# Optimization experiments

Hardware: AMD Instinct MI355X
Metric: run time of the kernel (lower is better)

Reference implementation:

```python
import jax, jax.numpy as jnp
import numpy as np

B, S, DM, H = 4, 2048, 512, 8
HD = DM // H


def setup_inputs() -> dict:
    key = jax.random.key(0)
    ks = jax.random.split(key, 12)
    x = jax.random.normal(ks[0], (B, S, DM), dtype=jnp.float32)
    # causal lower-triangular mask [B, S, S]
    mask = jnp.broadcast_to(jnp.tril(jnp.ones((S, S), dtype=jnp.int32)), (B, S, S))
    # sorted irregular day offsets (trading-day-like), in days
    days_offset = jnp.sort(
        jax.random.uniform(ks[1], (B, S), dtype=jnp.float32) * 3000.0, axis=-1
    )
    scale = 1.0 / np.sqrt(DM)
    Wq = jax.random.normal(ks[2], (DM, DM), dtype=jnp.float32) * scale
    bq = jnp.zeros((DM,), dtype=jnp.float32)
    Wk = jax.random.normal(ks[3], (DM, DM), dtype=jnp.float32) * scale
    bk = jnp.zeros((DM,), dtype=jnp.float32)
    Wv = jax.random.normal(ks[4], (DM, DM), dtype=jnp.float32) * scale
    bv = jnp.zeros((DM,), dtype=jnp.float32)
    Wo = jax.random.normal(ks[5], (DM, DM), dtype=jnp.float32) * scale
    bo = jnp.zeros((DM,), dtype=jnp.float32)
    decay_rate = jnp.float32(0.1)
    return {
        "x": x, "mask": mask, "days_offset": days_offset,
        "Wq": Wq, "bq": bq, "Wk": Wk, "bk": bk,
        "Wv": Wv, "bv": bv, "Wo": Wo, "bo": bo,
        "decay_rate": decay_rate,
    }


def reference(x, mask, days_offset, Wq, bq, Wk, bk, Wv, bv, Wo, bo, decay_rate):
    b, s, _ = x.shape
    # projections (torch Linear: x @ W.T + b), split heads -> [b, h, s, hd]
    def proj(W, bias):
        return (x @ W.T + bias).reshape(b, s, H, HD).transpose(0, 2, 1, 3)
    q, k, v = proj(Wq, bq), proj(Wk, bk), proj(Wv, bv)
    scores = jnp.einsum("bhqd,bhkd->bhqk", q, k) / jnp.sqrt(jnp.float32(HD))
    # temporal decay: exp(-rate * |t_i - t_j|), broadcast over heads
    dist = jnp.abs(days_offset[:, :, None] - days_offset[:, None, :])  # [b,s,s]
    decay = jnp.exp(-decay_rate * dist)
    scores = scores * decay[:, None, :, :]
    scores = jnp.where(mask[:, None, :, :] == 0, -jnp.inf, scores)
    attn = jax.nn.softmax(scores, axis=-1)  # dropout p=0 (eval)
    out = jnp.einsum("bhqk,bhkd->bhqd", attn, v)
    out = out.transpose(0, 2, 1, 3).reshape(b, s, DM)
    return out @ Wo.T + bo
```

## Files before the change

kernel.cpp:

```cpp
#include <hip/hip_runtime.h>
#include <hip/hip_fp16.h>


#define S_LEN 2048
#define DMODEL 512
#define NH 8
#define HD 64

typedef _Float16 half8 __attribute__((ext_vector_type(8)));
typedef _Float16 half4 __attribute__((ext_vector_type(4)));
typedef float floatx4 __attribute__((ext_vector_type(4)));

__device__ __forceinline__ void gload16(const _Float16* g, _Float16* l) {
    __builtin_amdgcn_global_load_lds(
        (const __attribute__((address_space(1))) void*)g,
        (__attribute__((address_space(3))) void*)l, 16, 0, 0);
}

__global__ __launch_bounds__(256) void cast_f32_f16(
    const float* __restrict__ x,
    const float* __restrict__ Wq, const float* __restrict__ Wk,
    const float* __restrict__ Wv, const float* __restrict__ Wo,
    _Float16* __restrict__ xh, _Float16* __restrict__ Wh)
{
    int i = blockIdx.x * 256 + threadIdx.x;
    const float* src; _Float16* dst; int off;
    if (i < 1048576) { src = x; dst = xh; off = i; }
    else {
        int j = i - 1048576;
        int w = j >> 16;
        int within = j & 65535;
        src = (w == 0) ? Wq : (w == 1) ? Wk : (w == 2) ? Wv : Wo;
        dst = Wh + w * (DMODEL * DMODEL);
        off = within;
    }
    float4 v = ((const float4*)src)[off];
    half4 h;
    h.x = (_Float16)v.x; h.y = (_Float16)v.y; h.z = (_Float16)v.z; h.w = (_Float16)v.w;
    *(half4*)(dst + (size_t)off * 4) = h;
}

template <int MODE>
__global__ __launch_bounds__(256) void gemm_k(
    const _Float16* __restrict__ A, const _Float16* __restrict__ Wbase,
    const float* __restrict__ b0, const float* __restrict__ b1,
    const float* __restrict__ b2,
    _Float16* __restrict__ outh, float* __restrict__ outf)
{
    __shared__ _Float16 As[128 * 64];
    __shared__ _Float16 Ws[128 * 64];
    __shared__ char epbuf[MODE == 0 ? (4 * 16 * 72 * 2) : (4 * 16 * 68 * 4)];
    const int t = threadIdx.x;
    const int bm = blockIdx.x, bn = blockIdx.y, z = blockIdx.z;
    const _Float16* Wp = Wbase + (MODE == 0 ? z * (DMODEL * DMODEL) : 0);
    const float* bias = (MODE == 0) ? (z == 0 ? b0 : (z == 1 ? b1 : b2)) : b0;
    const int w = t >> 6, lane = t & 63, l15 = lane & 15, quad = lane >> 4;
    const int wrow = (w >> 1) * 64, wcol = (w & 1) * 64;
    const int lrow = lane >> 3;
    const int sw = (lane & 7) ^ lrow;

    floatx4 acc[4][4] = {};
    for (int kb = 0; kb < 8; ++kb) {
        __syncthreads();
        #pragma unroll
        for (int i = 0; i < 4; ++i) {
            int row0 = w * 32 + i * 8;
            gload16(A  + (size_t)(bm * 128 + row0 + lrow) * DMODEL + kb * 64 + sw * 8, &As[row0 * 64]);
            gload16(Wp + (size_t)(bn * 128 + row0 + lrow) * DMODEL + kb * 64 + sw * 8, &Ws[row0 * 64]);
        }
        __syncthreads();
        #pragma unroll
        for (int kk = 0; kk < 2; ++kk) {
            half8 af[4], bf[4];
            #pragma unroll
            for (int mt = 0; mt < 4; ++mt)
                af[mt] = *(const half8*)(&As[(wrow + mt * 16 + l15) * 64 + (((quad + 4 * kk) ^ (l15 & 7)) * 8)]);
            #pragma unroll
            for (int nt = 0; nt < 4; ++nt)
                bf[nt] = *(const half8*)(&Ws[(wcol + nt * 16 + l15) * 64 + (((quad + 4 * kk) ^ (l15 & 7)) * 8)]);
            #pragma unroll
            for (int mt = 0; mt < 4; ++mt)
                #pragma unroll
                for (int nt = 0; nt < 4; ++nt)
                    acc[mt][nt] = __builtin_amdgcn_mfma_f32_16x16x32_f16(af[mt], bf[nt], acc[mt][nt], 0, 0, 0);
        }
    }

    if (MODE == 0 && z == 2) {
        #pragma unroll
        for (int mt = 0; mt < 4; ++mt)
            #pragma unroll
            for (int nt = 0; nt < 4; ++nt) {
                int n = bn * 128 + wcol + nt * 16 + l15;
                float bvv = bias[n];
                int m0 = bm * 128 + wrow + mt * 16 + quad * 4;
                int b = m0 >> 11, s0 = m0 & 2047;
                int hh = n >> 6, hd = n & 63;
                half4 hv;
                #pragma unroll
                for (int r = 0; r < 4; ++r) hv[r] = (_Float16)(acc[mt][nt][r] + bvv);
                *(half4*)(outh + (size_t)2 * (8192 * 512) +
                          ((size_t)(b * NH + hh) * HD + hd) * S_LEN + s0) = hv;
            }
    } else {
        float bv4[4];
        #pragma unroll
        for (int nt = 0; nt < 4; ++nt) bv4[nt] = bias[bn * 128 + wcol + nt * 16 + l15];
        const int rr = lane >> 3, cc = (lane & 7) ^ rr;
        if (MODE == 0) {
            _Float16* Ep = (_Float16*)epbuf + w * (16 * 72);
            const int hq = (bn * 128 + wcol) >> 6;
            #pragma unroll
            for (int mt = 0; mt < 4; ++mt) {
                #pragma unroll
                for (int nt = 0; nt < 4; ++nt)
                    #pragma unroll
                    for (int r = 0; r < 4; ++r)
                        Ep[(quad * 4 + r) * 72 + nt * 16 + l15] = (_Float16)(acc[mt][nt][r] + bv4[nt]);
                #pragma unroll
                for (int i2 = 0; i2 < 2; ++i2) {
                    int row = i2 * 8 + rr;
                    half8 v = *(const half8*)(&Ep[row * 72 + cc * 8]);
                    int m = bm * 128 + wrow + mt * 16 + row;
                    int bb = m >> 11, ss = m & 2047;
                    *(half8*)(outh + (size_t)z * (8192 * 512) +
                              ((size_t)(bb * NH + hq) * S_LEN + ss) * HD + cc * 8) = v;
                }
            }
        } else {
            float* Epf = (float*)epbuf + w * (16 * 68);
            #pragma unroll
            for (int mt = 0; mt < 4; ++mt) {
                #pragma unroll
                for (int nt = 0; nt < 4; ++nt)
                    #pragma unroll
                    for (int r = 0; r < 4; ++r)
                        Epf[(quad * 4 + r) * 68 + nt * 16 + l15] = acc[mt][nt][r] + bv4[nt];
                #pragma unroll
                for (int i2 = 0; i2 < 4; ++i2) {
                    int row = (i2 & 1) * 8 + rr;
                    int ch = cc + (i2 >> 1) * 8;
                    float4 v = *(const float4*)(&Epf[row * 68 + ch * 4]);
                    int m = bm * 128 + wrow + mt * 16 + row;
                    *(float4*)(outf + (size_t)m * DMODEL + bn * 128 + wcol + ch * 4) = v;
                }
            }
        }
    }
}

__global__ __launch_bounds__(256, 2) void attn_k(
    const _Float16* __restrict__ Qh, const _Float16* __restrict__ Kh,
    const _Float16* __restrict__ Vt, const float* __restrict__ days,
    const float* __restrict__ rate_p, _Float16* __restrict__ Ah)
{
    __shared__ _Float16 Ks[2][64 * 64];
    __shared__ _Float16 Vs[2][64 * 64];
    __shared__ float    eks[2][64];
    __shared__ _Float16 Ps[4][16 * 64];

    const int pr = blockIdx.x, h = blockIdx.y, b = blockIdx.z;
    const int t = threadIdx.x, w = t >> 6, lane = t & 63, l15 = lane & 15, quad = lane >> 4;
    const float rate = rate_p[0];
    const size_t bhoff = (size_t)(b * NH + h) * (size_t)(S_LEN * HD);
    const _Float16* Qb = Qh + bhoff;
    const _Float16* Kb = Kh + bhoff;
    const _Float16* Vb = Vt + bhoff;
    const float* daysb = days + b * S_LEN;
    const int lrow = lane >> 3, sw = (lane & 7) ^ lrow;
    const int e7 = l15 & 7;

    auto stage = [&](int kt, int buf) {
        #pragma unroll
        for (int i = 0; i < 2; ++i) {
            int grp = w * 2 + i;
            int row = grp * 8 + lrow;
            gload16(Kb + (size_t)(kt * 64 + row) * HD + sw * 8, &Ks[buf][grp * 512]);
            gload16(Vb + (size_t)row * S_LEN + kt * 64 + sw * 8, &Vs[buf][grp * 512]);
        }
        if (w == 0) {
            float tk0 = daysb[kt * 64];
            float d = daysb[kt * 64 + lane];
            eks[buf][lane] = __expf(fminf(rate * (d - tk0), 80.f));
        }
    };

    auto run_phase = [&](int j, int par0, int nextj) -> int {
        const int qg = j * 64 + w * 16 + l15;
        half8 qf0 = *(const half8*)(Qb + (size_t)qg * HD + quad * 8);
        half8 qf1 = *(const half8*)(Qb + (size_t)qg * HD + 32 + quad * 8);
        const float tq = daysb[qg];
        floatx4 oacc[4] = {};
        float lacc = 0.f;

        for (int kt = 0; kt <= j; ++kt) {
            const int par = (par0 + kt) & 1;
            __syncthreads();
            if (kt < j) stage(kt + 1, par ^ 1);
            else if (nextj >= 0) stage(0, par ^ 1);
            const float tk0 = daysb[kt * 64];
            half8 kf[4][2];
            #pragma unroll
            for (int c = 0; c < 4; ++c)
                #pragma unroll
                for (int kk = 0; kk < 2; ++kk)
                    kf[c][kk] = *(const half8*)(&Ks[par][(c * 16 + l15) * 64 + (((quad + 4 * kk) ^ e7) * 8)]);
            floatx4 sc[4];
            #pragma unroll
            for (int c = 0; c < 4; ++c) {
                floatx4 z4 = {};
                z4 = __builtin_amdgcn_mfma_f32_16x16x32_f16(kf[c][0], qf0, z4, 0, 0, 0);
                sc[c] = __builtin_amdgcn_mfma_f32_16x16x32_f16(kf[c][1], qf1, z4, 0, 0, 0);
            }
            half8 vf[4][2];
            #pragma unroll
            for (int s4 = 0; s4 < 4; ++s4)
                #pragma unroll
                for (int kk = 0; kk < 2; ++kk)
                    vf[s4][kk] = *(const half8*)(&Vs[par][(s4 * 16 + l15) * 64 + (((quad + 4 * kk) ^ e7) * 8)]);
            floatx4 ekv[4];
            #pragma unroll
            for (int c = 0; c < 4; ++c)
                ekv[c] = *(const floatx4*)(&eks[par][c * 16 + quad * 4]);
            const float eq = 0.125f * __expf(-rate * (tq - tk0));
            const bool dg = (kt == j);
            #pragma unroll
            for (int c = 0; c < 4; ++c) {
                float pvv[4];
                #pragma unroll
                for (int r = 0; r < 4; ++r) {
                    float sv = sc[c][r] * (eq * ekv[c][r]);
                    float p = __expf(sv - 2.0f);
                    if (dg && (kt * 64 + c * 16 + quad * 4 + r) > qg) p = 0.f;
                    lacc += p;
                    pvv[r] = p;
                }
                half4 hv;
                hv.x = (_Float16)pvv[0]; hv.y = (_Float16)pvv[1];
                hv.z = (_Float16)pvv[2]; hv.w = (_Float16)pvv[3];
                *(half4*)(&Ps[w][l15 * 64 + (((2 * c + (quad >> 1)) ^ e7) * 8) + (quad & 1) * 4]) = hv;
            }
            half8 pf0 = *(const half8*)(&Ps[w][l15 * 64 + ((quad ^ e7) * 8)]);
            half8 pf1 = *(const half8*)(&Ps[w][l15 * 64 + (((4 + quad) ^ e7) * 8)]);
            #pragma unroll
            for (int s4 = 0; s4 < 4; ++s4) {
                oacc[s4] = __builtin_amdgcn_mfma_f32_16x16x32_f16(vf[s4][0], pf0, oacc[s4], 0, 0, 0);
                oacc[s4] = __builtin_amdgcn_mfma_f32_16x16x32_f16(vf[s4][1], pf1, oacc[s4], 0, 0, 0);
            }
        }

        float l = lacc;
        l += __shfl_xor(l, 16);
        l += __shfl_xor(l, 32);
        float linv = 1.0f / l;
        #pragma unroll
        for (int s4 = 0; s4 < 4; ++s4) {
            half4 hv;
            #pragma unroll
            for (int r = 0; r < 4; ++r) hv[r] = (_Float16)(oacc[s4][r] * linv);
            *(half4*)(Ah + ((size_t)(b * S_LEN) + qg) * DMODEL + h * HD + s4 * 16 + quad * 4) = hv;
        }
        return (par0 + j + 1) & 1;
    };

    const int j0 = pr, j1 = 31 - pr;
    stage(0, 0);
    int p1 = run_phase(j0, 0, j1);
    run_phase(j1, p1, -1);
}

extern "C" void kernel_launch(void* const* d_in, const int* in_sizes, int n_in,
                              void* d_out, int out_size, void* d_ws, size_t ws_size,
                              hipStream_t stream)
{
    const float* x    = (const float*)d_in[0];
    const float* days = (const float*)d_in[2];
    const float* Wq   = (const float*)d_in[3];
    const float* bq   = (const float*)d_in[4];
    const float* Wk   = (const float*)d_in[5];
    const float* bk   = (const float*)d_in[6];
    const float* Wv   = (const float*)d_in[7];
    const float* bv   = (const float*)d_in[8];
    const float* Wo   = (const float*)d_in[9];
    const float* bo   = (const float*)d_in[10];
    const float* rate = (const float*)d_in[11];
    float* out = (float*)d_out;

    _Float16* xh = (_Float16*)d_ws;
    _Float16* Wh = xh + 4194304;
    _Float16* Qh = Wh + 1048576;
    _Float16* Kh = Qh + 4194304;
    _Float16* Vh = Kh + 4194304;
    _Float16* Ah = Vh + 4194304;

    cast_f32_f16<<<5120, 256, 0, stream>>>(x, Wq, Wk, Wv, Wo, xh, Wh);

    dim3 g0(64, 4, 3);
    gemm_k<0><<<g0, 256, 0, stream>>>(xh, Wh, bq, bk, bv, Qh, nullptr);

    dim3 ga(16, NH, 4);
    attn_k<<<ga, 256, 0, stream>>>(Qh, Kh, Vh, days, rate, Ah);

    dim3 g1(64, 4, 1);
    gemm_k<1><<<g1, 256, 0, stream>>>(Ah, Wh + 3 * (DMODEL * DMODEL), bo, bo, bo, nullptr, out);
}
```

Baseline: 206.9 us.

## Fuse fp32-to-fp16 cast into GEMM staging and reorder attention grid

```diff
diff --git a/kernel.cpp b/kernel.cpp
--- a/kernel.cpp
+++ b/kernel.cpp
@@ -17,47 +17,36 @@
         (__attribute__((address_space(3))) void*)l, 16, 0, 0);
 }
 
-__global__ __launch_bounds__(256) void cast_f32_f16(
+__device__ __forceinline__ void stage_f32(
+    const float* __restrict__ src, _Float16* __restrict__ dstbase,
+    int row0, int lrow, int sw, int lane7, int kcol)
+{
+    const float* p = src + (size_t)(row0 + lrow) * DMODEL + kcol + sw * 8;
+    float4 a = *(const float4*)p;
+    float4 b = *(const float4*)(p + 4);
+    half8 h;
+    h[0] = (_Float16)a.x; h[1] = (_Float16)a.y; h[2] = (_Float16)a.z; h[3] = (_Float16)a.w;
+    h[4] = (_Float16)b.x; h[5] = (_Float16)b.y; h[6] = (_Float16)b.z; h[7] = (_Float16)b.w;
+    *(half8*)(dstbase + (row0 + lrow) * 64 + lane7 * 8) = h;
+}
+
+__global__ __launch_bounds__(256) void qkv_gemm(
     const float* __restrict__ x,
-    const float* __restrict__ Wq, const float* __restrict__ Wk,
-    const float* __restrict__ Wv, const float* __restrict__ Wo,
-    _Float16* __restrict__ xh, _Float16* __restrict__ Wh)
-{
-    int i = blockIdx.x * 256 + threadIdx.x;
-    const float* src; _Float16* dst; int off;
-    if (i < 1048576) { src = x; dst = xh; off = i; }
-    else {
-        int j = i - 1048576;
-        int w = j >> 16;
-        int within = j & 65535;
-        src = (w == 0) ? Wq : (w == 1) ? Wk : (w == 2) ? Wv : Wo;
-        dst = Wh + w * (DMODEL * DMODEL);
-        off = within;
-    }
-    float4 v = ((const float4*)src)[off];
-    half4 h;
-    h.x = (_Float16)v.x; h.y = (_Float16)v.y; h.z = (_Float16)v.z; h.w = (_Float16)v.w;
-    *(half4*)(dst + (size_t)off * 4) = h;
-}
-
-template <int MODE>
-__global__ __launch_bounds__(256) void gemm_k(
-    const _Float16* __restrict__ A, const _Float16* __restrict__ Wbase,
-    const float* __restrict__ b0, const float* __restrict__ b1,
-    const float* __restrict__ b2,
-    _Float16* __restrict__ outh, float* __restrict__ outf)
+    const float* __restrict__ Wq, const float* __restrict__ Wk, const float* __restrict__ Wv,
+    const float* __restrict__ bq, const float* __restrict__ bk, const float* __restrict__ bv,
+    _Float16* __restrict__ outh)
 {
     __shared__ _Float16 As[128 * 64];
     __shared__ _Float16 Ws[128 * 64];
-    __shared__ char epbuf[MODE == 0 ? (4 * 16 * 72 * 2) : (4 * 16 * 68 * 4)];
+    __shared__ _Float16 Ep[4][16 * 72];
     const int t = threadIdx.x;
     const int bm = blockIdx.x, bn = blockIdx.y, z = blockIdx.z;
-    const _Float16* Wp = Wbase + (MODE == 0 ? z * (DMODEL * DMODEL) : 0);
-    const float* bias = (MODE == 0) ? (z == 0 ? b0 : (z == 1 ? b1 : b2)) : b0;
+    const float* Wp = (z == 0) ? Wq : (z == 1) ? Wk : Wv;
+    const float* bias = (z == 0) ? bq : (z == 1) ? bk : bv;
     const int w = t >> 6, lane = t & 63, l15 = lane & 15, quad = lane >> 4;
     const int wrow = (w >> 1) * 64, wcol = (w & 1) * 64;
-    const int lrow = lane >> 3;
-    const int sw = (lane & 7) ^ lrow;
+    const int lrow = lane >> 3, lane7 = lane & 7;
+    const int sw = lane7 ^ lrow;
 
     floatx4 acc[4][4] = {};
     for (int kb = 0; kb < 8; ++kb) {
@@ -65,8 +54,8 @@
         #pragma unroll
         for (int i = 0; i < 4; ++i) {
             int row0 = w * 32 + i * 8;
-            gload16(A  + (size_t)(bm * 128 + row0 + lrow) * DMODEL + kb * 64 + sw * 8, &As[row0 * 64]);
-            gload16(Wp + (size_t)(bn * 128 + row0 + lrow) * DMODEL + kb * 64 + sw * 8, &Ws[row0 * 64]);
+            stage_f32(x  + (size_t)(bm * 128) * DMODEL, As, row0, lrow, sw, lane7, kb * 64);
+            stage_f32(Wp + (size_t)(bn * 128) * DMODEL, Ws, row0, lrow, sw, lane7, kb * 64);
         }
         __syncthreads();
         #pragma unroll
@@ -86,7 +75,7 @@
         }
     }
 
-    if (MODE == 0 && z == 2) {
+    if (z == 2) {
         #pragma unroll
         for (int mt = 0; mt < 4; ++mt)
             #pragma unroll
@@ -107,44 +96,88 @@
         #pragma unroll
         for (int nt = 0; nt < 4; ++nt) bv4[nt] = bias[bn * 128 + wcol + nt * 16 + l15];
         const int rr = lane >> 3, cc = (lane & 7) ^ rr;
-        if (MODE == 0) {
-            _Float16* Ep = (_Float16*)epbuf + w * (16 * 72);
-            const int hq = (bn * 128 + wcol) >> 6;
-            #pragma unroll
-            for (int mt = 0; mt < 4; ++mt) {
+        _Float16* E = Ep[w];
+        const int hq = (bn * 128 + wcol) >> 6;
+        #pragma unroll
+        for (int mt = 0; mt < 4; ++mt) {
+            #pragma unroll
+            for (int nt = 0; nt < 4; ++nt)
+                #pragma unroll
+                for (int r = 0; r < 4; ++r)
+                    E[(quad * 4 + r) * 72 + nt * 16 + l15] = (_Float16)(acc[mt][nt][r] + bv4[nt]);
+            #pragma unroll
+            for (int i2 = 0; i2 < 2; ++i2) {
+                int row = i2 * 8 + rr;
+                half8 v = *(const half8*)(&E[row * 72 + cc * 8]);
+                int m = bm * 128 + wrow + mt * 16 + row;
+                int bb = m >> 11, ss = m & 2047;
+                *(half8*)(outh + (size_t)z * (8192 * 512) +
+                          ((size_t)(bb * NH + hq) * S_LEN + ss) * HD + cc * 8) = v;
+            }
+        }
+    }
+}
+
+__global__ __launch_bounds__(256) void out_gemm(
+    const _Float16* __restrict__ A, const float* __restrict__ Wo,
+    const float* __restrict__ bo, float* __restrict__ outf)
+{
+    __shared__ _Float16 As[128 * 64];
+    __shared__ _Float16 Ws[128 * 64];
+    __shared__ float Epf[4][16 * 68];
+    const int t = threadIdx.x;
+    const int bm = blockIdx.x, bn = blockIdx.y;
+    const int w = t >> 6, lane = t & 63, l15 = lane & 15, quad = lane >> 4;
+    const int wrow = (w >> 1) * 64, wcol = (w & 1) * 64;
+    const int lrow = lane >> 3, lane7 = lane & 7;
+    const int sw = lane7 ^ lrow;
+
+    floatx4 acc[4][4] = {};
+    for (int kb = 0; kb < 8; ++kb) {
+        __syncthreads();
+        #pragma unroll
+        for (int i = 0; i < 4; ++i) {
+            int row0 = w * 32 + i * 8;
+            gload16(A + (size_t)(bm * 128 + row0 + lrow) * DMODEL + kb * 64 + sw * 8, &As[row0 * 64]);
+            stage_f32(Wo + (size_t)(bn * 128) * DMODEL, Ws, row0, lrow, sw, lane7, kb * 64);
+        }
+        __syncthreads();
+        #pragma unroll
+        for (int kk = 0; kk < 2; ++kk) {
+            half8 af[4], bf[4];
+            #pragma unroll
+            for (int mt = 0; mt < 4; ++mt)
+                af[mt] = *(const half8*)(&As[(wrow + mt * 16 + l15) * 64 + (((quad + 4 * kk) ^ (l15 & 7)) * 8)]);
+            #pragma unroll
+            for (int nt = 0; nt < 4; ++nt)
+                bf[nt] = *(const half8*)(&Ws[(wcol + nt * 16 + l15) * 64 + (((quad + 4 * kk) ^ (l15 & 7)) * 8)]);
+            #pragma unroll
+            for (int mt = 0; mt < 4; ++mt)
                 #pragma unroll
                 for (int nt = 0; nt < 4; ++nt)
-                    #pragma unroll
-                    for (int r = 0; r < 4; ++r)
-                        Ep[(quad * 4 + r) * 72 + nt * 16 + l15] = (_Float16)(acc[mt][nt][r] + bv4[nt]);
-                #pragma unroll
-                for (int i2 = 0; i2 < 2; ++i2) {
-                    int row = i2 * 8 + rr;
-                    half8 v = *(const half8*)(&Ep[row * 72 + cc * 8]);
-                    int m = bm * 128 + wrow + mt * 16 + row;
-                    int bb = m >> 11, ss = m & 2047;
-                    *(half8*)(outh + (size_t)z * (8192 * 512) +
-                              ((size_t)(bb * NH + hq) * S_LEN + ss) * HD + cc * 8) = v;
-                }
-            }
-        } else {
-            float* Epf = (float*)epbuf + w * (16 * 68);
-            #pragma unroll
-            for (int mt = 0; mt < 4; ++mt) {
-                #pragma unroll
-                for (int nt = 0; nt < 4; ++nt)
-                    #pragma unroll
-                    for (int r = 0; r < 4; ++r)
-                        Epf[(quad * 4 + r) * 68 + nt * 16 + l15] = acc[mt][nt][r] + bv4[nt];
-                #pragma unroll
-                for (int i2 = 0; i2 < 4; ++i2) {
-                    int row = (i2 & 1) * 8 + rr;
-                    int ch = cc + (i2 >> 1) * 8;
-                    float4 v = *(const float4*)(&Epf[row * 68 + ch * 4]);
-                    int m = bm * 128 + wrow + mt * 16 + row;
-                    *(float4*)(outf + (size_t)m * DMODEL + bn * 128 + wcol + ch * 4) = v;
-                }
-            }
+                    acc[mt][nt] = __builtin_amdgcn_mfma_f32_16x16x32_f16(af[mt], bf[nt], acc[mt][nt], 0, 0, 0);
+        }
+    }
+
+    float bv4[4];
+    #pragma unroll
+    for (int nt = 0; nt < 4; ++nt) bv4[nt] = bo[bn * 128 + wcol + nt * 16 + l15];
+    const int rr = lane >> 3, cc = (lane & 7) ^ rr;
+    float* E = Epf[w];
+    #pragma unroll
+    for (int mt = 0; mt < 4; ++mt) {
+        #pragma unroll
+        for (int nt = 0; nt < 4; ++nt)
+            #pragma unroll
+            for (int r = 0; r < 4; ++r)
+                E[(quad * 4 + r) * 68 + nt * 16 + l15] = acc[mt][nt][r] + bv4[nt];
+        #pragma unroll
+        for (int i2 = 0; i2 < 4; ++i2) {
+            int row = (i2 & 1) * 8 + rr;
+            int ch = cc + (i2 >> 1) * 8;
+            float4 v = *(const float4*)(&E[row * 68 + ch * 4]);
+            int m = bm * 128 + wrow + mt * 16 + row;
+            *(float4*)(outf + (size_t)m * DMODEL + bn * 128 + wcol + ch * 4) = v;
         }
     }
 }
@@ -159,7 +192,7 @@
     __shared__ float    eks[2][64];
     __shared__ _Float16 Ps[4][16 * 64];
 
-    const int pr = blockIdx.x, h = blockIdx.y, b = blockIdx.z;
+    const int h = blockIdx.x, pr = blockIdx.y, b = blockIdx.z;
     const int t = threadIdx.x, w = t >> 6, lane = t & 63, l15 = lane & 15, quad = lane >> 4;
     const float rate = rate_p[0];
     const size_t bhoff = (size_t)(b * NH + h) * (size_t)(S_LEN * HD);
@@ -286,21 +319,17 @@
     const float* rate = (const float*)d_in[11];
     float* out = (float*)d_out;
 
-    _Float16* xh = (_Float16*)d_ws;
-    _Float16* Wh = xh + 4194304;
-    _Float16* Qh = Wh + 1048576;
+    _Float16* Qh = (_Float16*)d_ws;
     _Float16* Kh = Qh + 4194304;
     _Float16* Vh = Kh + 4194304;
     _Float16* Ah = Vh + 4194304;
 
-    cast_f32_f16<<<5120, 256, 0, stream>>>(x, Wq, Wk, Wv, Wo, xh, Wh);
-
     dim3 g0(64, 4, 3);
-    gemm_k<0><<<g0, 256, 0, stream>>>(xh, Wh, bq, bk, bv, Qh, nullptr);
-
-    dim3 ga(16, NH, 4);
+    qkv_gemm<<<g0, 256, 0, stream>>>(x, Wq, Wk, Wv, bq, bk, bv, Qh);
+
+    dim3 ga(NH, 16, 4);
     attn_k<<<ga, 256, 0, stream>>>(Qh, Kh, Vh, days, rate, Ah);
 
     dim3 g1(64, 4, 1);
-    gemm_k<1><<<g1, 256, 0, stream>>>(Ah, Wh + 3 * (DMODEL * DMODEL), bo, bo, bo, nullptr, out);
-}
+    out_gemm<<<g1, 256, 0, stream>>>(Ah, Wo, bo, out);
+}
```

Result: slower. 211.4 us (+2.2%).
